# Optimization experiments

Measured on AMD Instinct MI355X. Metric: run time of the kernel, lower is better.

Reference implementation:

```python
import jax, jax.numpy as jnp
import numpy as np

HEADS = 8


def setup_inputs() -> dict:
    key = jax.random.key(0)
    k1, k2, k3 = jax.random.split(key, 3)
    b, n, d = 4, 2048, 256
    x = jax.random.normal(k1, (b, n, d), dtype=jnp.float32)
    # torch Linear weight is [out, in]; we store transposed [in, out] for x @ W
    w_qkv = jax.random.normal(k2, (d, 3 * d), dtype=jnp.float32) * (d ** -0.5)
    b_qkv = jnp.zeros((3 * d,), dtype=jnp.float32)
    w_out = jax.random.normal(k3, (d, d), dtype=jnp.float32) * (d ** -0.5)
    b_out = jnp.zeros((d,), dtype=jnp.float32)
    return {"x": x, "w_qkv": w_qkv, "b_qkv": b_qkv, "w_out": w_out, "b_out": b_out}


def reference(x, w_qkv, b_qkv, w_out, b_out):
    b, n, d = x.shape
    h = HEADS
    dh = d // h
    scale = d ** -0.5  # NOTE: original scales by full dim**-0.5, not head_dim
    qkv = x @ w_qkv + b_qkv                      # [b, n, 3d]
    q, k, v = jnp.split(qkv, 3, axis=-1)         # each [b, n, d]
    to_heads = lambda t: t.reshape(b, n, h, dh).transpose(0, 2, 1, 3)  # [b,h,n,dh]
    q, k, v = to_heads(q), to_heads(k), to_heads(v)
    dots = jnp.einsum('bhid,bhjd->bhij', q, k) * scale   # [b,h,n,n]
    attn = jax.nn.softmax(dots, axis=-1)
    out = jnp.einsum('bhij,bhjd->bhid', attn, v)         # [b,h,n,dh]
    out = out.transpose(0, 2, 1, 3).reshape(b, n, d)     # [b,n,d]
    return out @ w_out + b_out  # dropout is identity in eval mode
```

## Files before the change

kernel.cpp:

```cpp
#include <hip/hip_runtime.h>
#include <hip/hip_bf16.h>
#include <math.h>

#define BATCH  4
#define SEQ    2048
#define DMODEL 256
#define NH     8
#define DH     32
#define MTOT   (BATCH*SEQ)
#define QSCALE 0.09016844005556021f

typedef short  bf16x8 __attribute__((ext_vector_type(8)));
typedef float  f32x4  __attribute__((ext_vector_type(4)));

static __device__ __forceinline__ ushort f2bf(float f) {
    __hip_bfloat16 h = __float2bfloat16(f);
    return __builtin_bit_cast(ushort, h);
}
static __device__ __forceinline__ uint rne2(float a, float b) {
    uint ua = __builtin_bit_cast(uint, a);
    uint ub = __builtin_bit_cast(uint, b);
    ua += 0x7FFFu + ((ua >> 16) & 1u);
    ub += 0x7FFFu + ((ub >> 16) & 1u);
    return __builtin_amdgcn_perm(ub, ua, 0x07060302);
}
static __device__ __forceinline__ uint pk2(float a, float b) {
#if __has_builtin(__builtin_amdgcn_cvt_pk_bf16_f32)
    auto r = __builtin_amdgcn_cvt_pk_bf16_f32(a, b);
    return __builtin_bit_cast(uint, r);
#else
    return rne2(a, b);
#endif
}

#define LSQ 72
#define KS_STRIDE 40
#define VT_STRIDE 136

__global__ __launch_bounds__(256) void wcvt_all(
    const float* __restrict__ wq, const float* __restrict__ wo,
    const float* __restrict__ x,
    ushort* __restrict__ wqT, ushort* __restrict__ woT,
    ushort* __restrict__ xbf)
{
    const int t  = threadIdx.x;
    const int bx = blockIdx.x;
    if (bx >= 32) {
        const size_t base = ((size_t)(bx - 32) * 8 + blockIdx.y) * 4096 + t * 16;
        float4 f0 = *(const float4*)(x + base);
        float4 f1 = *(const float4*)(x + base + 4);
        float4 f2 = *(const float4*)(x + base + 8);
        float4 f3 = *(const float4*)(x + base + 12);
        uint4 w0, w1;
        w0.x = pk2(f0.x, f0.y); w0.y = pk2(f0.z, f0.w);
        w0.z = pk2(f1.x, f1.y); w0.w = pk2(f1.z, f1.w);
        w1.x = pk2(f2.x, f2.y); w1.y = pk2(f2.z, f2.w);
        w1.z = pk2(f3.x, f3.y); w1.w = pk2(f3.z, f3.w);
        *(uint4*)&xbf[base]     = w0;
        *(uint4*)&xbf[base + 8] = w1;
        return;
    }
    __shared__ float T[32][33];
    const float* w; ushort* wT; int N, n0;
    if (bx < 24) { w = wq; wT = wqT; N = 768; n0 = bx * 32; }
    else         { w = wo; wT = woT; N = 256; n0 = (bx - 24) * 32; }
    const int k0 = blockIdx.y * 32;
    {
        int tr = t >> 3, tc = (t & 7) * 4;
        *(float4*)&T[tr][tc] = *(const float4*)(w + (size_t)(k0 + tr) * N + n0 + tc);
    }
    __syncthreads();
    int nl = t >> 3, kq = (t & 7) * 4;
    ushort4 pk;
    pk.x = f2bf(T[kq + 0][nl]); pk.y = f2bf(T[kq + 1][nl]);
    pk.z = f2bf(T[kq + 2][nl]); pk.w = f2bf(T[kq + 3][nl]);
    *(ushort4*)&wT[(size_t)(n0 + nl) * 256 + k0 + kq] = pk;
}

__global__ __launch_bounds__(256, 3) void qkv_gemm(
    const ushort* __restrict__ xb_, const ushort* __restrict__ wT,
    const float* __restrict__ bias,
    ushort* __restrict__ qo, ushort* __restrict__ ko, ushort* __restrict__ vo)
{
    __shared__ ushort As[64 * LSQ];
    __shared__ ushort Bs[128 * LSQ];
    const int tid  = threadIdx.x;
    const int wid  = tid >> 6;
    const int lane = tid & 63;
    const int lq   = lane & 15;
    const int quad = lane >> 4;
    const int wm   = wid & 1;
    const int wn   = wid >> 1;
    const int m0   = blockIdx.y * 64;
    const int n0   = blockIdx.x * 128;
    const bool isV = (blockIdx.x >= 4);

    const int ar0 = tid >> 3,         ac0 = (tid & 7) * 8;
    const int ar1 = (tid + 256) >> 3;
    const int br0 = tid >> 3,         bc0 = (tid & 7) * 8;
    const int br1 = (tid + 256) >> 3;
    const int br2 = (tid + 512) >> 3;
    const int br3 = (tid + 768) >> 3;

    const ushort* xb = xb_ + (size_t)m0 * 256;
    const ushort* wb = wT  + (size_t)n0 * 256;

    f32x4 acc[8];
#pragma unroll
    for (int i = 0; i < 8; ++i) acc[i] = {0.f, 0.f, 0.f, 0.f};

    uint4 ra0 = *(const uint4*)(xb + (size_t)ar0 * 256 + ac0);
    uint4 ra1 = *(const uint4*)(xb + (size_t)ar1 * 256 + ac0);
    uint4 rb0 = *(const uint4*)(wb + (size_t)br0 * 256 + bc0);
    uint4 rb1 = *(const uint4*)(wb + (size_t)br1 * 256 + bc0);
    uint4 rb2 = *(const uint4*)(wb + (size_t)br2 * 256 + bc0);
    uint4 rb3 = *(const uint4*)(wb + (size_t)br3 * 256 + bc0);

    for (int k0 = 0; k0 < 256; k0 += 64) {
        __syncthreads();
        *(uint4*)&As[ar0 * LSQ + ac0] = ra0;
        *(uint4*)&As[ar1 * LSQ + ac0] = ra1;
        *(uint4*)&Bs[br0 * LSQ + bc0] = rb0;
        *(uint4*)&Bs[br1 * LSQ + bc0] = rb1;
        *(uint4*)&Bs[br2 * LSQ + bc0] = rb2;
        *(uint4*)&Bs[br3 * LSQ + bc0] = rb3;
        __syncthreads();

        const int kn = (k0 + 64) & 255;
        ra0 = *(const uint4*)(xb + (size_t)ar0 * 256 + kn + ac0);
        ra1 = *(const uint4*)(xb + (size_t)ar1 * 256 + kn + ac0);
        rb0 = *(const uint4*)(wb + (size_t)br0 * 256 + kn + bc0);
        rb1 = *(const uint4*)(wb + (size_t)br1 * 256 + kn + bc0);
        rb2 = *(const uint4*)(wb + (size_t)br2 * 256 + kn + bc0);
        rb3 = *(const uint4*)(wb + (size_t)br3 * 256 + kn + bc0);

#pragma unroll
        for (int kh = 0; kh < 2; ++kh) {
            bf16x8 af[2], bfg[4];
#pragma unroll
            for (int mi = 0; mi < 2; ++mi)
                af[mi]  = *(const bf16x8*)&As[(wm * 32 + mi * 16 + lq) * LSQ + kh * 32 + quad * 8];
#pragma unroll
            for (int ni = 0; ni < 4; ++ni)
                bfg[ni] = *(const bf16x8*)&Bs[(wn * 64 + ni * 16 + lq) * LSQ + kh * 32 + quad * 8];
            if (isV) {
#pragma unroll
                for (int mi = 0; mi < 2; ++mi)
#pragma unroll
                    for (int ni = 0; ni < 4; ++ni)
                        acc[mi * 4 + ni] = __builtin_amdgcn_mfma_f32_16x16x32_bf16(
                            af[mi], bfg[ni], acc[mi * 4 + ni], 0, 0, 0);
            } else {
#pragma unroll
                for (int ni = 0; ni < 4; ++ni)
#pragma unroll
                    for (int mi = 0; mi < 2; ++mi)
                        acc[ni * 2 + mi] = __builtin_amdgcn_mfma_f32_16x16x32_bf16(
                            bfg[ni], af[mi], acc[ni * 2 + mi], 0, 0, 0);
            }
        }
    }

    if (!isV) {
#pragma unroll
        for (int ni = 0; ni < 4; ++ni) {
            int nb = n0 + wn * 64 + ni * 16 + quad * 4;
            float4 bs = *(const float4*)(bias + nb);
            int h   = (nb >> 5) & 7;
            int dh0 = nb & 31;
            bool  isQ = (nb < 256);
            float sc  = isQ ? QSCALE : 1.0f;
            ushort* dst = isQ ? qo : ko;
#pragma unroll
            for (int mi = 0; mi < 2; ++mi) {
                int m   = m0 + wm * 32 + mi * 16 + lq;
                int b   = m >> 11, seq = m & 2047;
                f32x4 c = acc[ni * 2 + mi];
                ushort4 pk;
                pk.x = f2bf((c[0] + bs.x) * sc); pk.y = f2bf((c[1] + bs.y) * sc);
                pk.z = f2bf((c[2] + bs.z) * sc); pk.w = f2bf((c[3] + bs.w) * sc);
                *(ushort4*)&dst[(((size_t)b * NH + h) * SEQ + seq) * DH + dh0] = pk;
            }
        }
    } else {
#pragma unroll
        for (int ni = 0; ni < 4; ++ni) {
            int n  = n0 + wn * 64 + ni * 16 + lq;
            int h  = (n >> 5) & 7;
            int dh = n & 31;
            float bsc = bias[n];
#pragma unroll
            for (int mi = 0; mi < 2; ++mi) {
                int mb  = m0 + wm * 32 + mi * 16 + quad * 4;
                int b   = mb >> 11, seq = mb & 2047;
                f32x4 c = acc[mi * 4 + ni];
                ushort4 pk;
                pk.x = f2bf(c[0] + bsc); pk.y = f2bf(c[1] + bsc);
                pk.z = f2bf(c[2] + bsc); pk.w = f2bf(c[3] + bsc);
                *(ushort4*)&vo[(((size_t)b * NH + h) * DH + dh) * SEQ + seq] = pk;
            }
        }
    }
}

__global__ __launch_bounds__(256, 2) void attn_mfma(
    const ushort* __restrict__ qb, const ushort* __restrict__ kb,
    const ushort* __restrict__ vtb, ushort* __restrict__ a_bf)
{
    __shared__ ushort Ks[128 * KS_STRIDE];
    __shared__ ushort VsT[32 * VT_STRIDE];

    const int tid  = threadIdx.x;
    const int wid  = tid >> 6;
    const int lane = tid & 63;
    const int lq   = lane & 15;
    const int quad = lane >> 4;

    const int lin = blockIdx.x + (blockIdx.y << 4) + (blockIdx.z << 7);
    const int swz = ((lin & 7) << 6) | (lin >> 3);
    const int h   = (swz >> 4) & 7;
    const int b   = swz >> 7;
    const int bh  = b * NH + h;
    const int q0  = (swz & 15) * 128 + wid * 32;

    const ushort* qbase = qb + ((size_t)bh * SEQ + q0) * DH;
    const bf16x8 qf0 = *(const bf16x8*)(qbase + (size_t)lq * DH + quad * 8);
    const bf16x8 qf1 = *(const bf16x8*)(qbase + (size_t)(16 + lq) * DH + quad * 8);

    const ushort* kbase  = kb  + (size_t)bh * SEQ * DH;
    const ushort* vtbase = vtb + (size_t)bh * DH * SEQ;

    const int f0 = tid, f1 = tid + 256;
    const int kgo0 = (f0 >> 2) * DH + (f0 & 3) * 8;
    const int kgo1 = (f1 >> 2) * DH + (f1 & 3) * 8;
    const int klo0 = (f0 >> 2) * KS_STRIDE + (f0 & 3) * 8;
    const int klo1 = (f1 >> 2) * KS_STRIDE + (f1 & 3) * 8;
    const int vgo0 = (f0 >> 4) * SEQ + (f0 & 15) * 8;
    const int vgo1 = (f1 >> 4) * SEQ + (f1 & 15) * 8;
    const int vlo0 = (f0 >> 4) * VT_STRIDE + (f0 & 15) * 8;
    const int vlo1 = (f1 >> 4) * VT_STRIDE + (f1 & 15) * 8;

    uint4 kr0 = *(const uint4*)(kbase  + kgo0);
    uint4 kr1 = *(const uint4*)(kbase  + kgo1);
    uint4 vr0 = *(const uint4*)(vtbase + vgo0);
    uint4 vr1 = *(const uint4*)(vtbase + vgo1);

    f32x4 o0 = {0.f,0.f,0.f,0.f}, o1 = {0.f,0.f,0.f,0.f};
    f32x4 o2 = {0.f,0.f,0.f,0.f}, o3 = {0.f,0.f,0.f,0.f};
    f32x4 la0 = {0.f,0.f,0.f,0.f}, la1 = {0.f,0.f,0.f,0.f};
    const bf16x8 ones = {0x3F80, 0x3F80, 0x3F80, 0x3F80,
                         0x3F80, 0x3F80, 0x3F80, 0x3F80};

    for (int kt = 0; kt < SEQ; kt += 128) {
        __syncthreads();
        *(uint4*)&Ks[klo0]  = kr0;
        *(uint4*)&Ks[klo1]  = kr1;
        *(uint4*)&VsT[vlo0] = vr0;
        *(uint4*)&VsT[vlo1] = vr1;
        __syncthreads();

        {
            const int ktn = (kt + 128) & (SEQ - 1);
            const ushort* kn = kbase  + (size_t)ktn * DH;
            const ushort* vn = vtbase + ktn;
            kr0 = *(const uint4*)(kn + kgo0);
            kr1 = *(const uint4*)(kn + kgo1);
            vr0 = *(const uint4*)(vn + vgo0);
            vr1 = *(const uint4*)(vn + vgo1);
        }

        f32x4 st0[8], st1[8];
#pragma unroll
        for (int t = 0; t < 8; ++t) {
            bf16x8 kf = *(const bf16x8*)&Ks[(t * 16 + lq) * KS_STRIDE + quad * 8];
            f32x4 z = {0.f, 0.f, 0.f, 0.f};
            st0[t] = __builtin_amdgcn_mfma_f32_16x16x32_bf16(kf, qf0, z, 0, 0, 0);
            st1[t] = __builtin_amdgcn_mfma_f32_16x16x32_bf16(kf, qf1, z, 0, 0, 0);
        }

#pragma unroll
        for (int s = 0; s < 4; ++s) {
            bf16x8 v0 = *(const bf16x8*)&VsT[lq        * VT_STRIDE + s * 32 + quad * 8];
            bf16x8 v1 = *(const bf16x8*)&VsT[(16 + lq) * VT_STRIDE + s * 32 + quad * 8];

            bf16x8 p0, p1;
            {
                f32x4 a = st0[2 * s], c = st0[2 * s + 1];
                uint t0lo = pk2(__builtin_amdgcn_exp2f(a[0]), __builtin_amdgcn_exp2f(a[1]));
                uint t0hi = pk2(__builtin_amdgcn_exp2f(a[2]), __builtin_amdgcn_exp2f(a[3]));
                uint t1lo = pk2(__builtin_amdgcn_exp2f(c[0]), __builtin_amdgcn_exp2f(c[1]));
                uint t1hi = pk2(__builtin_amdgcn_exp2f(c[2]), __builtin_amdgcn_exp2f(c[3]));
#if __has_builtin(__builtin_amdgcn_permlane32_swap) && __has_builtin(__builtin_amdgcn_permlane16_swap)
                auto rl = __builtin_amdgcn_permlane32_swap(t0lo, t1lo, false, false);
                auto rh = __builtin_amdgcn_permlane32_swap(t0hi, t1hi, false, false);
                auto sl = __builtin_amdgcn_permlane16_swap(rl[0], rl[1], false, false);
                auto sh = __builtin_amdgcn_permlane16_swap(rh[0], rh[1], false, false);
                uint4 pw = {sl[0], sh[0], sl[1], sh[1]};
#else
                uint a0 = __shfl_xor((int)t0lo, 32), b0 = __shfl_xor((int)t1lo, 32);
                uint a1 = __shfl_xor((int)t0hi, 32), b1 = __shfl_xor((int)t1hi, 32);
                uint Xl = (lane & 32) ? b0 : t0lo,  Yl = (lane & 32) ? t1lo : a0;
                uint Xh = (lane & 32) ? b1 : t0hi,  Yh = (lane & 32) ? t1hi : a1;
                uint sXl = __shfl_xor((int)Xl, 16), sYl = __shfl_xor((int)Yl, 16);
                uint sXh = __shfl_xor((int)Xh, 16), sYh = __shfl_xor((int)Yh, 16);
                uint4 pw = {(lane & 16) ? sYl : Xl, (lane & 16) ? sYh : Xh,
                            (lane & 16) ? Yl : sXl, (lane & 16) ? Yh : sXh};
#endif
                p0 = __builtin_bit_cast(bf16x8, pw);
            }
            {
                f32x4 a = st1[2 * s], c = st1[2 * s + 1];
                uint t0lo = pk2(__builtin_amdgcn_exp2f(a[0]), __builtin_amdgcn_exp2f(a[1]));
                uint t0hi = pk2(__builtin_amdgcn_exp2f(a[2]), __builtin_amdgcn_exp2f(a[3]));
                uint t1lo = pk2(__builtin_amdgcn_exp2f(c[0]), __builtin_amdgcn_exp2f(c[1]));
                uint t1hi = pk2(__builtin_amdgcn_exp2f(c[2]), __builtin_amdgcn_exp2f(c[3]));
#if __has_builtin(__builtin_amdgcn_permlane32_swap) && __has_builtin(__builtin_amdgcn_permlane16_swap)
                auto rl = __builtin_amdgcn_permlane32_swap(t0lo, t1lo, false, false);
                auto rh = __builtin_amdgcn_permlane32_swap(t0hi, t1hi, false, false);
                auto sl = __builtin_amdgcn_permlane16_swap(rl[0], rl[1], false, false);
                auto sh = __builtin_amdgcn_permlane16_swap(rh[0], rh[1], false, false);
                uint4 pw = {sl[0], sh[0], sl[1], sh[1]};
#else
                uint a0 = __shfl_xor((int)t0lo, 32), b0 = __shfl_xor((int)t1lo, 32);
                uint a1 = __shfl_xor((int)t0hi, 32), b1 = __shfl_xor((int)t1hi, 32);
                uint Xl = (lane & 32) ? b0 : t0lo,  Yl = (lane & 32) ? t1lo : a0;
                uint Xh = (lane & 32) ? b1 : t0hi,  Yh = (lane & 32) ? t1hi : a1;
                uint sXl = __shfl_xor((int)Xl, 16), sYl = __shfl_xor((int)Yl, 16);
                uint sXh = __shfl_xor((int)Xh, 16), sYh = __shfl_xor((int)Yh, 16);
                uint4 pw = {(lane & 16) ? sYl : Xl, (lane & 16) ? sYh : Xh,
                            (lane & 16) ? Yl : sXl, (lane & 16) ? Yh : sXh};
#endif
                p1 = __builtin_bit_cast(bf16x8, pw);
            }

            o0  = __builtin_amdgcn_mfma_f32_16x16x32_bf16(v0,   p0, o0,  0, 0, 0);
            o1  = __builtin_amdgcn_mfma_f32_16x16x32_bf16(v1,   p0, o1,  0, 0, 0);
            o2  = __builtin_amdgcn_mfma_f32_16x16x32_bf16(v0,   p1, o2,  0, 0, 0);
            o3  = __builtin_amdgcn_mfma_f32_16x16x32_bf16(v1,   p1, o3,  0, 0, 0);
            la0 = __builtin_amdgcn_mfma_f32_16x16x32_bf16(ones, p0, la0, 0, 0, 0);
            la1 = __builtin_amdgcn_mfma_f32_16x16x32_bf16(ones, p1, la1, 0, 0, 0);
        }
    }

    float inv0 = 1.0f / la0[0];
    float inv1 = 1.0f / la1[0];
    ushort* dst0 = a_bf + ((size_t)b * SEQ + q0 + lq) * DMODEL + h * DH;
    ushort* dst1 = dst0 + 16 * DMODEL;
    uint2 w0, w1;
    w0.x = pk2(o0[0] * inv0, o0[1] * inv0);
    w0.y = pk2(o0[2] * inv0, o0[3] * inv0);
    w1.x = pk2(o1[0] * inv0, o1[1] * inv0);
    w1.y = pk2(o1[2] * inv0, o1[3] * inv0);
    *(uint2*)&dst0[quad * 4]      = w0;
    *(uint2*)&dst0[16 + quad * 4] = w1;
    w0.x = pk2(o2[0] * inv1, o2[1] * inv1);
    w0.y = pk2(o2[2] * inv1, o2[3] * inv1);
    w1.x = pk2(o3[0] * inv1, o3[1] * inv1);
    w1.y = pk2(o3[2] * inv1, o3[3] * inv1);
    *(uint2*)&dst1[quad * 4]      = w0;
    *(uint2*)&dst1[16 + quad * 4] = w1;
}

__global__ __launch_bounds__(256) void out_gemm(
    const ushort* __restrict__ a, const ushort* __restrict__ wT,
    const float* __restrict__ bias, float* __restrict__ out)
{
    __shared__ ushort As[64 * LSQ];
    __shared__ ushort Bs[64 * LSQ];
    const int tid  = threadIdx.x;
    const int wid  = tid >> 6;
    const int lane = tid & 63;
    const int lq   = lane & 15;
    const int quad = lane >> 4;
    const int wm   = wid & 1;
    const int wn   = wid >> 1;
    const int m0   = blockIdx.y * 64;
    const int n0   = blockIdx.x * 64;

    const int f0 = tid, f1 = tid + 256;
    const int r0 = f0 >> 3, c0 = (f0 & 7) * 8;
    const int r1 = f1 >> 3, c1 = (f1 & 7) * 8;

    const ushort* ab = a  + (size_t)m0 * 256;
    const ushort* wb = wT + (size_t)n0 * 256;

    f32x4 acc[4];
#pragma unroll
    for (int i = 0; i < 4; ++i) acc[i] = {0.f, 0.f, 0.f, 0.f};

    uint4 ra0 = *(const uint4*)(ab + (size_t)r0 * 256 + c0);
    uint4 ra1 = *(const uint4*)(ab + (size_t)r1 * 256 + c1);
    uint4 rb0 = *(const uint4*)(wb + (size_t)r0 * 256 + c0);
    uint4 rb1 = *(const uint4*)(wb + (size_t)r1 * 256 + c1);

    for (int k0 = 0; k0 < 256; k0 += 64) {
        __syncthreads();
        *(uint4*)&As[r0 * LSQ + c0] = ra0;
        *(uint4*)&As[r1 * LSQ + c1] = ra1;
        *(uint4*)&Bs[r0 * LSQ + c0] = rb0;
        *(uint4*)&Bs[r1 * LSQ + c1] = rb1;
        __syncthreads();

        const int kn = (k0 + 64) & 255;
        ra0 = *(const uint4*)(ab + (size_t)r0 * 256 + kn + c0);
        ra1 = *(const uint4*)(ab + (size_t)r1 * 256 + kn + c1);
        rb0 = *(const uint4*)(wb + (size_t)r0 * 256 + kn + c0);
        rb1 = *(const uint4*)(wb + (size_t)r1 * 256 + kn + c1);

#pragma unroll
        for (int kh = 0; kh < 2; ++kh) {
            bf16x8 af[2], bfg[2];
#pragma unroll
            for (int mi = 0; mi < 2; ++mi)
                af[mi]  = *(const bf16x8*)&As[(wm * 32 + mi * 16 + lq) * LSQ + kh * 32 + quad * 8];
#pragma unroll
            for (int ni = 0; ni < 2; ++ni)
                bfg[ni] = *(const bf16x8*)&Bs[(wn * 32 + ni * 16 + lq) * LSQ + kh * 32 + quad * 8];
#pragma unroll
            for (int ni = 0; ni < 2; ++ni)
#pragma unroll
                for (int mi = 0; mi < 2; ++mi)
                    acc[ni * 2 + mi] = __builtin_amdgcn_mfma_f32_16x16x32_bf16(
                        bfg[ni], af[mi], acc[ni * 2 + mi], 0, 0, 0);
        }
    }

#pragma unroll
    for (int ni = 0; ni < 2; ++ni) {
        int nb = n0 + wn * 32 + ni * 16 + quad * 4;
        float4 bs = *(const float4*)(bias + nb);
#pragma unroll
        for (int mi = 0; mi < 2; ++mi) {
            int m = m0 + wm * 32 + mi * 16 + lq;
            f32x4 c = acc[ni * 2 + mi];
            float4 o;
            o.x = c[0] + bs.x; o.y = c[1] + bs.y;
            o.z = c[2] + bs.z; o.w = c[3] + bs.w;
            *(float4*)&out[(size_t)m * DMODEL + nb] = o;
        }
    }
}

extern "C" void kernel_launch(void* const* d_in, const int* in_sizes, int n_in,
                              void* d_out, int out_size, void* d_ws, size_t ws_size,
                              hipStream_t stream) {
    const float* x     = (const float*)d_in[0];
    const float* w_qkv = (const float*)d_in[1];
    const float* b_qkv = (const float*)d_in[2];
    const float* w_out = (const float*)d_in[3];
    const float* b_out = (const float*)d_in[4];
    float* out = (float*)d_out;

    const size_t TSZ = (size_t)MTOT * DMODEL;
    ushort* q_ws = (ushort*)d_ws;
    ushort* k_ws = q_ws + TSZ;
    ushort* v_ws = k_ws + TSZ;
    ushort* a_bf = v_ws + TSZ;
    ushort* xbf  = a_bf + TSZ;
    ushort* wqT  = xbf + TSZ;
    ushort* woT  = wqT + 768 * 256;

    wcvt_all<<<dim3(96, 8), 256, 0, stream>>>(w_qkv, w_out, x, wqT, woT, xbf);
    qkv_gemm<<<dim3(6, 128), 256, 0, stream>>>(xbf, wqT, b_qkv, q_ws, k_ws, v_ws);
    attn_mfma<<<dim3(SEQ / 128, NH, BATCH), 256, 0, stream>>>(
        q_ws, k_ws, v_ws, a_bf);
    out_gemm<<<dim3(4, 128), 256, 0, stream>>>(a_bf, woT, b_out, out);
}
```

Measured before the change: 123.5 us.

## Split attention KV sequence across two wave groups with LDS reduction

Doubles the attention block to 512 threads. Each half of the waves processes alternating 128-key tiles of a 256-key step for the same query rows. The two halves merge their partial output and row-sum accumulators through shared memory before normalizing and storing. This is meant to raise wave occupancy and latency hiding, since the grid has only 512 blocks. In exchange it adds a final LDS reduction, extra barriers and more shared memory per block. It relies on no running max being used, so partial sums add directly.

```diff
diff --git a/kernel.cpp b/kernel.cpp
--- a/kernel.cpp
+++ b/kernel.cpp
@@ -203,25 +203,30 @@
     }
 }
 
-__global__ __launch_bounds__(256, 2) void attn_mfma(
+__global__ __launch_bounds__(512, 4) void attn_mfma(
     const ushort* __restrict__ qb, const ushort* __restrict__ kb,
     const ushort* __restrict__ vtb, ushort* __restrict__ a_bf)
 {
-    __shared__ ushort Ks[128 * KS_STRIDE];
-    __shared__ ushort VsT[32 * VT_STRIDE];
+    __shared__ ushort KsA[128 * KS_STRIDE];
+    __shared__ ushort KsB[128 * KS_STRIDE];
+    __shared__ ushort VsA[32 * VT_STRIDE];
+    __shared__ ushort VsB[32 * VT_STRIDE];
+    __shared__ float  Red[4][64][20];
 
     const int tid  = threadIdx.x;
     const int wid  = tid >> 6;
     const int lane = tid & 63;
     const int lq   = lane & 15;
     const int quad = lane >> 4;
+    const int half = wid >> 2;
+    const int wq   = wid & 3;
 
     const int lin = blockIdx.x + (blockIdx.y << 4) + (blockIdx.z << 7);
     const int swz = ((lin & 7) << 6) | (lin >> 3);
     const int h   = (swz >> 4) & 7;
     const int b   = swz >> 7;
     const int bh  = b * NH + h;
-    const int q0  = (swz & 15) * 128 + wid * 32;
+    const int q0  = (swz & 15) * 128 + wq * 32;
 
     const ushort* qbase = qb + ((size_t)bh * SEQ + q0) * DH;
     const bf16x8 qf0 = *(const bf16x8*)(qbase + (size_t)lq * DH + quad * 8);
@@ -230,20 +235,18 @@
     const ushort* kbase  = kb  + (size_t)bh * SEQ * DH;
     const ushort* vtbase = vtb + (size_t)bh * DH * SEQ;
 
-    const int f0 = tid, f1 = tid + 256;
-    const int kgo0 = (f0 >> 2) * DH + (f0 & 3) * 8;
-    const int kgo1 = (f1 >> 2) * DH + (f1 & 3) * 8;
-    const int klo0 = (f0 >> 2) * KS_STRIDE + (f0 & 3) * 8;
-    const int klo1 = (f1 >> 2) * KS_STRIDE + (f1 & 3) * 8;
-    const int vgo0 = (f0 >> 4) * SEQ + (f0 & 15) * 8;
-    const int vgo1 = (f1 >> 4) * SEQ + (f1 & 15) * 8;
-    const int vlo0 = (f0 >> 4) * VT_STRIDE + (f0 & 15) * 8;
-    const int vlo1 = (f1 >> 4) * VT_STRIDE + (f1 & 15) * 8;
-
-    uint4 kr0 = *(const uint4*)(kbase  + kgo0);
-    uint4 kr1 = *(const uint4*)(kbase  + kgo1);
-    uint4 vr0 = *(const uint4*)(vtbase + vgo0);
-    uint4 vr1 = *(const uint4*)(vtbase + vgo1);
+    const int kgo = (tid >> 2) * DH + (tid & 3) * 8;
+    const int klo = (tid >> 2) * KS_STRIDE + (tid & 3) * 8;
+    const int vgo = (tid >> 4) * SEQ + (tid & 15) * 8;
+    const int vlo = (tid >> 4) * VT_STRIDE + (tid & 15) * 8;
+
+    uint4 krA = *(const uint4*)(kbase  + kgo);
+    uint4 vrA = *(const uint4*)(vtbase + vgo);
+    uint4 krB = *(const uint4*)(kbase  + 128 * DH + kgo);
+    uint4 vrB = *(const uint4*)(vtbase + 128 + vgo);
+
+    const ushort* Ksw = half ? KsB : KsA;
+    const ushort* Vsw = half ? VsB : VsA;
 
     f32x4 o0 = {0.f,0.f,0.f,0.f}, o1 = {0.f,0.f,0.f,0.f};
     f32x4 o2 = {0.f,0.f,0.f,0.f}, o3 = {0.f,0.f,0.f,0.f};
@@ -251,28 +254,27 @@
     const bf16x8 ones = {0x3F80, 0x3F80, 0x3F80, 0x3F80,
                          0x3F80, 0x3F80, 0x3F80, 0x3F80};
 
-    for (int kt = 0; kt < SEQ; kt += 128) {
-        __syncthreads();
-        *(uint4*)&Ks[klo0]  = kr0;
-        *(uint4*)&Ks[klo1]  = kr1;
-        *(uint4*)&VsT[vlo0] = vr0;
-        *(uint4*)&VsT[vlo1] = vr1;
+    for (int kt = 0; kt < SEQ; kt += 256) {
+        __syncthreads();
+        *(uint4*)&KsA[klo] = krA;
+        *(uint4*)&VsA[vlo] = vrA;
+        *(uint4*)&KsB[klo] = krB;
+        *(uint4*)&VsB[vlo] = vrB;
         __syncthreads();
 
         {
-            const int ktn = (kt + 128) & (SEQ - 1);
-            const ushort* kn = kbase  + (size_t)ktn * DH;
-            const ushort* vn = vtbase + ktn;
-            kr0 = *(const uint4*)(kn + kgo0);
-            kr1 = *(const uint4*)(kn + kgo1);
-            vr0 = *(const uint4*)(vn + vgo0);
-            vr1 = *(const uint4*)(vn + vgo1);
+            const int ka = (kt + 256) & (SEQ - 1);
+            const int kbn = (kt + 384) & (SEQ - 1);
+            krA = *(const uint4*)(kbase  + (size_t)ka  * DH + kgo);
+            vrA = *(const uint4*)(vtbase + ka  + vgo);
+            krB = *(const uint4*)(kbase  + (size_t)kbn * DH + kgo);
+            vrB = *(const uint4*)(vtbase + kbn + vgo);
         }
 
         f32x4 st0[8], st1[8];
 #pragma unroll
         for (int t = 0; t < 8; ++t) {
-            bf16x8 kf = *(const bf16x8*)&Ks[(t * 16 + lq) * KS_STRIDE + quad * 8];
+            bf16x8 kf = *(const bf16x8*)&Ksw[(t * 16 + lq) * KS_STRIDE + quad * 8];
             f32x4 z = {0.f, 0.f, 0.f, 0.f};
             st0[t] = __builtin_amdgcn_mfma_f32_16x16x32_bf16(kf, qf0, z, 0, 0, 0);
             st1[t] = __builtin_amdgcn_mfma_f32_16x16x32_bf16(kf, qf1, z, 0, 0, 0);
@@ -280,8 +282,8 @@
 
 #pragma unroll
         for (int s = 0; s < 4; ++s) {
-            bf16x8 v0 = *(const bf16x8*)&VsT[lq        * VT_STRIDE + s * 32 + quad * 8];
-            bf16x8 v1 = *(const bf16x8*)&VsT[(16 + lq) * VT_STRIDE + s * 32 + quad * 8];
+            bf16x8 v0 = *(const bf16x8*)&Vsw[lq        * VT_STRIDE + s * 32 + quad * 8];
+            bf16x8 v1 = *(const bf16x8*)&Vsw[(16 + lq) * VT_STRIDE + s * 32 + quad * 8];
 
             bf16x8 p0, p1;
             {
@@ -342,23 +344,41 @@
         }
     }
 
-    float inv0 = 1.0f / la0[0];
-    float inv1 = 1.0f / la1[0];
-    ushort* dst0 = a_bf + ((size_t)b * SEQ + q0 + lq) * DMODEL + h * DH;
-    ushort* dst1 = dst0 + 16 * DMODEL;
-    uint2 w0, w1;
-    w0.x = pk2(o0[0] * inv0, o0[1] * inv0);
-    w0.y = pk2(o0[2] * inv0, o0[3] * inv0);
-    w1.x = pk2(o1[0] * inv0, o1[1] * inv0);
-    w1.y = pk2(o1[2] * inv0, o1[3] * inv0);
-    *(uint2*)&dst0[quad * 4]      = w0;
-    *(uint2*)&dst0[16 + quad * 4] = w1;
-    w0.x = pk2(o2[0] * inv1, o2[1] * inv1);
-    w0.y = pk2(o2[2] * inv1, o2[3] * inv1);
-    w1.x = pk2(o3[0] * inv1, o3[1] * inv1);
-    w1.y = pk2(o3[2] * inv1, o3[3] * inv1);
-    *(uint2*)&dst1[quad * 4]      = w0;
-    *(uint2*)&dst1[16 + quad * 4] = w1;
+    __syncthreads();
+    if (half) {
+        float* r = &Red[wq][lane][0];
+        r[0]  = o0[0]; r[1]  = o0[1]; r[2]  = o0[2]; r[3]  = o0[3];
+        r[4]  = o1[0]; r[5]  = o1[1]; r[6]  = o1[2]; r[7]  = o1[3];
+        r[8]  = o2[0]; r[9]  = o2[1]; r[10] = o2[2]; r[11] = o2[3];
+        r[12] = o3[0]; r[13] = o3[1]; r[14] = o3[2]; r[15] = o3[3];
+        r[16] = la0[0]; r[17] = la1[0];
+    }
+    __syncthreads();
+    if (!half) {
+        const float* r = &Red[wq][lane][0];
+        o0[0] += r[0];  o0[1] += r[1];  o0[2] += r[2];  o0[3] += r[3];
+        o1[0] += r[4];  o1[1] += r[5];  o1[2] += r[6];  o1[3] += r[7];
+        o2[0] += r[8];  o2[1] += r[9];  o2[2] += r[10]; o2[3] += r[11];
+        o3[0] += r[12]; o3[1] += r[13]; o3[2] += r[14]; o3[3] += r[15];
+        float inv0 = 1.0f / (la0[0] + r[16]);
+        float inv1 = 1.0f / (la1[0] + r[17]);
+
+        ushort* dst0 = a_bf + ((size_t)b * SEQ + q0 + lq) * DMODEL + h * DH;
+        ushort* dst1 = dst0 + 16 * DMODEL;
+        uint2 w0, w1;
+        w0.x = pk2(o0[0] * inv0, o0[1] * inv0);
+        w0.y = pk2(o0[2] * inv0, o0[3] * inv0);
+        w1.x = pk2(o1[0] * inv0, o1[1] * inv0);
+        w1.y = pk2(o1[2] * inv0, o1[3] * inv0);
+        *(uint2*)&dst0[quad * 4]      = w0;
+        *(uint2*)&dst0[16 + quad * 4] = w1;
+        w0.x = pk2(o2[0] * inv1, o2[1] * inv1);
+        w0.y = pk2(o2[2] * inv1, o2[3] * inv1);
+        w1.x = pk2(o3[0] * inv1, o3[1] * inv1);
+        w1.y = pk2(o3[2] * inv1, o3[3] * inv1);
+        *(uint2*)&dst1[quad * 4]      = w0;
+        *(uint2*)&dst1[16 + quad * 4] = w1;
+    }
 }
 
 __global__ __launch_bounds__(256) void out_gemm(
@@ -462,7 +482,7 @@
 
     wcvt_all<<<dim3(96, 8), 256, 0, stream>>>(w_qkv, w_out, x, wqT, woT, xbf);
     qkv_gemm<<<dim3(6, 128), 256, 0, stream>>>(xbf, wqT, b_qkv, q_ws, k_ws, v_ws);
-    attn_mfma<<<dim3(SEQ / 128, NH, BATCH), 256, 0, stream>>>(
+    attn_mfma<<<dim3(SEQ / 128, NH, BATCH), 512, 0, stream>>>(
         q_ws, k_ws, v_ws, a_bf);
     out_gemm<<<dim3(4, 128), 256, 0, stream>>>(a_bf, woT, b_out, out);
 }
```

Measured after the change: 137.9 us. +11.7%, slower.
